# Performance work log

Hardware: AMD Instinct MI355X
Metric: run time of the kernel (lower is better)

Reference implementation:

```python
import jax, jax.numpy as jnp
import numpy as np

P_SIZE = 128   # proto_size
HID = 768      # hidden_size
BATCH = 32
NREL = 16
RATIO = 0.5    # proto_emb_ratio


def setup_inputs() -> dict:
    key = jax.random.key(0)
    k1, k2, k3, k4 = jax.random.split(key, 4)
    return {
        "instance_embedding": jax.random.normal(k1, (BATCH, HID), jnp.float32),
        # small scale keeps sigmoid(p_h @ M_r @ p_t) away from hard saturation
        "relation_embedding": jax.random.normal(k2, (NREL, HID, HID), jnp.float32) * 0.02,
        "rel_label_ids": jax.random.randint(k3, (BATCH, NREL, P_SIZE), 0, P_SIZE + 1, dtype=jnp.int32),
        "labels": jnp.arange(BATCH, dtype=jnp.int32),  # distinct -> torch.unique is exact with static shapes
        "prototypes": jax.random.normal(k4, (P_SIZE, HID), jnp.float32),  # nn.Embedding weight
    }


def reference(instance_embedding, relation_embedding, rel_label_ids, labels, prototypes):
    P, H = prototypes.shape
    B, R, _ = rel_label_ids.shape

    # torch.unique(labels, return_inverse=True): sorted uniques + inverse map.
    labels_unique = jnp.sort(labels)                      # [K] (K == B, labels distinct)
    inv = jnp.argsort(jnp.argsort(labels))                # index_list (rank of each label)
    # original code: index = index_list[k] -> rel rows permuted by inverse map
    rel_k = rel_label_ids[inv]                            # [K,R,P]

    total_nonzero = jnp.sum(rel_label_ids) > 0
    batch_mask = (jnp.sum(rel_k, axis=(1, 2)) > 0)[:, None, None]   # skip if sum(rel[index])==0
    row_mask = (jnp.sum(rel_k, axis=2) > 0)[:, :, None]             # skip if sum(rel[index][i])==0
    m = (rel_k != P) & batch_mask & row_mask & total_nonzero        # [K,R,P] active entries
    mf = m.astype(prototypes.dtype)

    P0 = prototypes                                       # get_proto_embedding(): never updated inside loop
    heads = jnp.minimum(rel_k, P - 1)                     # safe gather (masked where == P)
    Ph = P0[heads]                                        # [K,R,P,H]  (largest intermediate)
    pt = P0[labels_unique]                                # [K,H]

    # sim[k,i,j] = sigmoid(P0[head] @ M_r[i] @ P0[label_k])
    v = jnp.einsum('rhg,kg->krh', relation_embedding, pt)           # [K,R,H]
    sim = jax.nn.sigmoid(jnp.einsum('krph,krh->krp', Ph, v))        # [K,R,P]

    # logits_ol init: zeros, then logits_ol[:][:][:][0] = 1.0 sets the k==0 slab to 1.0
    base = jnp.zeros((B, R, P, 2), prototypes.dtype).at[0].set(1.0)
    l1 = jnp.where(m, sim, base[..., 1])
    l0 = jnp.where(m, 1.0 - sim, base[..., 0])
    logits_ol = jnp.stack([l0, l1], axis=-1).reshape(-1, 2)         # [K*R*P, 2]
    labels_ol = m.astype(jnp.int32).reshape(-1)                     # [K*R*P]

    # proto propagation: mean over active (i,j) of P0[head] @ M_r[i]
    w = jnp.einsum('krp,krph->krh', mf, Ph)                         # [K,R,H]
    prop = jnp.einsum('krh,rhg->kg', w, relation_embedding)         # [K,H]
    n = jnp.sum(mf, axis=(1, 2))                                    # num_prop per k
    prop = prop / jnp.maximum(n, 1.0)[:, None]
    old_rows = prototypes[labels_unique]
    new_rows = RATIO * old_rows + (1.0 - RATIO) * prop
    rows = jnp.where((n > 0)[:, None], new_rows, old_rows)
    proto_embedding = prototypes.at[labels_unique].set(rows)        # scatter update (distinct rows)

    # CrossEntropyLoss (mean); 0 when all rel ids are zero (labels_ol would be None)
    logp = jax.nn.log_softmax(logits_ol, axis=-1)
    ce = -jnp.mean(jnp.take_along_axis(logp, labels_ol[:, None], axis=1))
    loss_ol = jnp.where(total_nonzero, ce, 0.0)

    # logits = -||proto - instance||^2 pairwise: [B, P]
    diff = instance_embedding[:, None, :] - proto_embedding[None, :, :]
    logits = -jnp.sum(diff * diff, axis=2)

    return logits, loss_ol, proto_embedding
```

## Files before the change

kernel.cpp:

```cpp
#include <hip/hip_runtime.h>
#include <hip/hip_bf16.h>
#include <math.h>

#define K_B 32
#define NRELD 16
#define PSZ 128
#define HID 768

using bf16x8 = __attribute__((ext_vector_type(8))) short;
using f32x4  = __attribute__((ext_vector_type(4))) float;

__device__ __forceinline__ unsigned int f2bf(float x) {
    unsigned int u = __float_as_uint(x);
    return (u + 0x7fffu + ((u >> 16) & 1u)) >> 16;
}
__device__ __forceinline__ float bf2f(unsigned short b) {
    return __uint_as_float(((unsigned int)b) << 16);
}

__global__ __launch_bounds__(192) void k_prep(
        const int* __restrict__ labels, const int* __restrict__ relIds,
        const float* __restrict__ P0,
        unsigned short* __restrict__ S_bf, unsigned short* __restrict__ P0_bf,
        unsigned short* __restrict__ P0T_bf, unsigned short* __restrict__ pt_bf,
        int* __restrict__ rowflag, int* __restrict__ cntRow,
        int* __restrict__ done)
{
    int bid = blockIdx.x, t = threadIdx.x;
    int k = bid >> 4, r = bid & 15;
    __shared__ int lab[32], rankS[32], luS[32], ownS[128];
    __shared__ int hist[128], redS[128];
    if (t < 32) lab[t] = labels[t];
    if (t < 128) { hist[t] = 0; ownS[t] = -1; }
    __syncthreads();
    if (t < 32) { int rk = 0; for (int j = 0; j < 32; ++j) rk += (lab[j] < lab[t]); rankS[t] = rk; }
    __syncthreads();
    if (t < 32) luS[rankS[t]] = lab[t];
    __syncthreads();
    if (t < 32) ownS[luS[t]] = t;
    __syncthreads();

    int id = 0, isv = 0;
    if (t < 128) {
        id = relIds[((size_t)rankS[k]*NRELD + r)*PSZ + t];
        isv = (id != PSZ);
        if (isv) atomicAdd(&hist[id], 1);
        redS[t] = id + (isv << 20);
    }
    __syncthreads();
    for (int off = 64; off; off >>= 1) {
        if (t < off && t < 128) redS[t] += redS[t + off];
        __syncthreads();
    }
    int rowsum = redS[0] & 0xFFFFF;
    int cnt    = redS[0] >> 20;
    int rf     = (rowsum > 0);
    if (t < 128)
        S_bf[(size_t)bid*128 + t] = (unsigned short)f2bf(rf ? (float)hist[t] : 0.f);
    if (t == 0) { rowflag[bid] = rf; cntRow[bid] = cnt; }
    if (bid == 0 && t == 0) done[0] = 0;

    if (bid < 128) {
        int p = bid;
        float4 v4 = *(const float4*)&P0[(size_t)p*HID + t*4];
        unsigned int b0 = f2bf(v4.x), b1 = f2bf(v4.y), b2 = f2bf(v4.z), b3 = f2bf(v4.w);
        uint2 d; d.x = b0 | (b1 << 16); d.y = b2 | (b3 << 16);
        *(uint2*)&P0_bf[(size_t)p*HID + t*4] = d;
        P0T_bf[(size_t)(t*4+0)*128 + p] = (unsigned short)b0;
        P0T_bf[(size_t)(t*4+1)*128 + p] = (unsigned short)b1;
        P0T_bf[(size_t)(t*4+2)*128 + p] = (unsigned short)b2;
        P0T_bf[(size_t)(t*4+3)*128 + p] = (unsigned short)b3;
        int kk = ownS[p];
        if (kk >= 0) *(uint2*)&pt_bf[(size_t)kk*HID + t*4] = d;
    }
}

__global__ __launch_bounds__(256) void k_vw(
        const float* __restrict__ rel, const unsigned short* __restrict__ pt_bf,
        const unsigned short* __restrict__ S_bf, const unsigned short* __restrict__ P0T_bf,
        unsigned short* __restrict__ v_bf, unsigned short* __restrict__ w_bf,
        float* __restrict__ prop, float* __restrict__ lossAcc)
{
    __shared__ unsigned short sh[32*768 + 64*128];
    int bid = blockIdx.x, t = threadIdx.x;
    int wave = t >> 6, lane = t & 63;

    if (bid < 192) {
        int r = bid & 15, hs = bid >> 4;
        unsigned short* ptS = sh;
        unsigned short* AS  = sh + 32*768;
        for (int i = t; i < 3072; i += 256) {
            int k = i / 96, c = i % 96;
            uint4 d = *(const uint4*)&pt_bf[(size_t)k*HID + c*8];
            *(uint4*)&ptS[k*768 + (c ^ (k & 7))*8] = d;
        }
        const int gq = (t & 31) * 4;
        const int hr = t >> 5;
        const size_t relbase = ((size_t)r*HID + hs*64) * HID;
        float4 buf[8];
        #pragma unroll
        for (int rr = 0; rr < 8; ++rr)
            buf[rr] = *(const float4*)&rel[relbase + (size_t)(hr + rr*8)*HID + gq];
        f32x4 acc[2] = {{0.f,0.f,0.f,0.f},{0.f,0.f,0.f,0.f}};
        const int arow = wave*16 + (lane & 15);
        for (int gt = 0; gt < 6; ++gt) {
            __syncthreads();
            #pragma unroll
            for (int rr = 0; rr < 8; ++rr) {
                int h_l = hr + rr*8;
                float4 v4 = buf[rr];
                int cs = (gq >> 3) ^ (h_l & 7);
                uint2 d; d.x = f2bf(v4.x) | (f2bf(v4.y) << 16);
                d.y = f2bf(v4.z) | (f2bf(v4.w) << 16);
                *(uint2*)&AS[h_l*128 + cs*8 + (gq & 4)] = d;
            }
            __syncthreads();
            if (gt < 5) {
                int gn = gt*128 + 128;
                #pragma unroll
                for (int rr = 0; rr < 8; ++rr)
                    buf[rr] = *(const float4*)&rel[relbase + (size_t)(hr + rr*8)*HID + gn + gq];
            }
            #pragma unroll
            for (int kk = 0; kk < 4; ++kk) {
                int cA = (kk*4 + (lane >> 4)) ^ (arow & 7);
                bf16x8 a = *(const bf16x8*)&AS[arow*128 + cA*8];
                #pragma unroll
                for (int nf = 0; nf < 2; ++nf) {
                    int k = nf*16 + (lane & 15);
                    int cB = (gt*16 + kk*4 + (lane >> 4)) ^ (k & 7);
                    bf16x8 b = *(const bf16x8*)&ptS[k*768 + cB*8];
                    acc[nf] = __builtin_amdgcn_mfma_f32_16x16x32_bf16(a, b, acc[nf], 0, 0, 0);
                }
            }
        }
        int h_out = hs*64 + wave*16 + (lane >> 4) * 4;
        #pragma unroll
        for (int nf = 0; nf < 2; ++nf) {
            int k = nf*16 + (lane & 15);
            uint2 d; d.x = f2bf(acc[nf][0]) | (f2bf(acc[nf][1]) << 16);
            d.y = f2bf(acc[nf][2]) | (f2bf(acc[nf][3]) << 16);
            *(uint2*)&v_bf[((size_t)k*NRELD + r)*HID + h_out] = d;
        }
    } else {
        int idx = bid - 192;
        int ms = idx / 12, ns = idx % 12;
        unsigned short* AS2 = sh;
        unsigned short* BS2 = sh + 64*128;
        if (t < 64) *(float4*)&prop[idx*256 + t*4] = float4{0.f,0.f,0.f,0.f};
        if (idx == 0 && t == 0) lossAcc[0] = 0.f;
        for (int i = t; i < 1024; i += 256) {
            int row = i >> 4, c = i & 15;
            *(uint4*)&AS2[row*128 + (c ^ (row & 7))*8] =
                *(const uint4*)&S_bf[(size_t)(ms*64 + row)*128 + c*8];
            *(uint4*)&BS2[row*128 + (c ^ (row & 7))*8] =
                *(const uint4*)&P0T_bf[(size_t)(ns*64 + row)*128 + c*8];
        }
        __syncthreads();
        f32x4 acc[4] = {{0.f,0.f,0.f,0.f},{0.f,0.f,0.f,0.f},{0.f,0.f,0.f,0.f},{0.f,0.f,0.f,0.f}};
        int arow = wave*16 + (lane & 15);
        #pragma unroll
        for (int kk = 0; kk < 4; ++kk) {
            int cA = (kk*4 + (lane >> 4)) ^ (arow & 7);
            bf16x8 a = *(const bf16x8*)&AS2[arow*128 + cA*8];
            #pragma unroll
            for (int nf = 0; nf < 4; ++nf) {
                int brow = nf*16 + (lane & 15);
                int cB = (kk*4 + (lane >> 4)) ^ (brow & 7);
                bf16x8 b = *(const bf16x8*)&BS2[brow*128 + cB*8];
                acc[nf] = __builtin_amdgcn_mfma_f32_16x16x32_bf16(a, b, acc[nf], 0, 0, 0);
            }
        }
        int kr0 = ms*64 + wave*16 + (lane >> 4) * 4;
        #pragma unroll
        for (int nf = 0; nf < 4; ++nf) {
            int h = ns*64 + nf*16 + (lane & 15);
            #pragma unroll
            for (int j = 0; j < 4; ++j)
                w_bf[(size_t)(kr0 + j)*HID + h] = (unsigned short)f2bf(acc[nf][j]);
        }
    }
}

__global__ __launch_bounds__(256) void k_prop_mfma(
        const float* __restrict__ rel, const unsigned short* __restrict__ w_bf,
        float* __restrict__ prop)
{
    int r = blockIdx.x, gs = blockIdx.y, t = threadIdx.x;
    int wave = t >> 6, lane = t & 63;
    __shared__ unsigned short WS[32*768];
    __shared__ unsigned short BS[64*128];
    for (int i = t; i < 3072; i += 256) {
        int k = i / 96, c = i % 96;
        uint4 d = *(const uint4*)&w_bf[((size_t)k*NRELD + r)*HID + c*8];
        *(uint4*)&WS[k*768 + (c ^ (k & 7))*8] = d;
    }
    const int gqq = t & 15;
    const int h4  = t >> 4;
    const size_t relb = (size_t)r*HID*HID + (size_t)gs*64;
    float4 buf[8];
    #pragma unroll
    for (int sup = 0; sup < 2; ++sup)
        #pragma unroll
        for (int rr = 0; rr < 4; ++rr)
            buf[sup*4+rr] = *(const float4*)&rel[relb + (size_t)(sup*64 + h4*4 + rr)*HID + gqq*4];
    f32x4 acc[2] = {{0.f,0.f,0.f,0.f},{0.f,0.f,0.f,0.f}};
    for (int ht = 0; ht < 6; ++ht) {
        __syncthreads();
        #pragma unroll
        for (int sup = 0; sup < 2; ++sup) {
            #pragma unroll
            for (int i = 0; i < 4; ++i) {
                int g_l = gqq*4 + i;
                int hloc = sup*64 + h4*4;
                unsigned int p0 = f2bf(((const float*)&buf[sup*4+0])[i]);
                unsigned int p1 = f2bf(((const float*)&buf[sup*4+1])[i]);
                unsigned int p2 = f2bf(((const float*)&buf[sup*4+2])[i]);
                unsigned int p3 = f2bf(((const float*)&buf[sup*4+3])[i]);
                int cs = (hloc >> 3) ^ ((g_l >> 2) & 7);
                uint2 d; d.x = p0 | (p1 << 16); d.y = p2 | (p3 << 16);
                *(uint2*)&BS[g_l*128 + cs*8 + (hloc & 4)] = d;
            }
        }
        __syncthreads();
        if (ht < 5) {
            int hn = ht*128 + 128;
            #pragma unroll
            for (int sup = 0; sup < 2; ++sup)
                #pragma unroll
                for (int rr = 0; rr < 4; ++rr)
                    buf[sup*4+rr] = *(const float4*)&rel[relb + (size_t)(hn + sup*64 + h4*4 + rr)*HID + gqq*4];
        }
        int g_l = wave*16 + (lane & 15);
        #pragma unroll
        for (int kk = 0; kk < 4; ++kk) {
            int cB = (kk*4 + (lane >> 4)) ^ ((g_l >> 2) & 7);
            bf16x8 b = *(const bf16x8*)&BS[g_l*128 + cB*8];
            #pragma unroll
            for (int mf = 0; mf < 2; ++mf) {
                int arow = mf*16 + (lane & 15);
                int cA = (ht*16 + kk*4 + (lane >> 4)) ^ (arow & 7);
                bf16x8 a = *(const bf16x8*)&WS[arow*768 + cA*8];
                acc[mf] = __builtin_amdgcn_mfma_f32_16x16x32_bf16(a, b, acc[mf], 0, 0, 0);
            }
        }
    }
    int gcol = gs*64 + wave*16 + (lane & 15);
    #pragma unroll
    for (int mf = 0; mf < 2; ++mf) {
        int k0 = mf*16 + (lane >> 4)*4;
        #pragma unroll
        for (int j = 0; j < 4; ++j)
            atomicAdd(&prop[(size_t)(k0 + j)*HID + gcol], acc[mf][j]);
    }
}

__global__ __launch_bounds__(256) void k_tail(
        const unsigned short* __restrict__ v_bf, const unsigned short* __restrict__ P0_bf,
        const unsigned short* __restrict__ S_bf, float* __restrict__ lossAcc,
        int* __restrict__ done,
        const float* __restrict__ P0, const float* __restrict__ prop,
        const int* __restrict__ rowflag, const int* __restrict__ cntRow,
        const int* __restrict__ labels, const float* __restrict__ inst,
        float* __restrict__ outProto, float* __restrict__ outLogits,
        float* __restrict__ outLoss)
{
    __shared__ __align__(16) char shraw[16*772*4];
    __shared__ int lab[32], rankS[32], luS[32], ownS[128];
    __shared__ float redF[256];
    __shared__ int redI[256];
    __shared__ float nActS[16];
    __shared__ int kS2[16];
    const int bid = blockIdx.x, t = threadIdx.x;
    const int wave = t >> 6, lane = t & 63;

    if (t < 32) lab[t] = labels[t];
    if (t < 128) ownS[t] = -1;
    __syncthreads();
    if (t < 32) { int rk = 0; for (int j = 0; j < 32; ++j) rk += (lab[j] < lab[t]); rankS[t] = rk; }
    __syncthreads();
    if (t < 32) luS[rankS[t]] = lab[t];
    __syncthreads();
    if (t < 32) ownS[luS[t]] = t;
    __syncthreads();

    if (bid < 32) {
        int ms = bid;
        unsigned short* AS  = (unsigned short*)shraw;
        unsigned short* BS2 = (unsigned short*)shraw + 16*128;
        f32x4 acc[2] = {{0.f,0.f,0.f,0.f},{0.f,0.f,0.f,0.f}};
        for (int ht = 0; ht < 6; ++ht) {
            int h0 = ht * 128;
            __syncthreads();
            {
                int row = t >> 4, c = t & 15;
                *(uint4*)&AS[row*128 + (c ^ (row & 7))*8] =
                    *(const uint4*)&v_bf[(size_t)(ms*16 + row)*HID + h0 + c*8];
                #pragma unroll
                for (int q = 0; q < 8; ++q) {
                    int j2 = t + q*256;
                    int prow = j2 >> 4, c2 = j2 & 15;
                    *(uint4*)&BS2[prow*128 + (c2 ^ (prow & 7))*8] =
                        *(const uint4*)&P0_bf[(size_t)prow*HID + h0 + c2*8];
                }
            }
            __syncthreads();
            int arow = lane & 15;
            #pragma unroll
            for (int kk = 0; kk < 4; ++kk) {
                int cA = (kk*4 + (lane >> 4)) ^ (arow & 7);
                bf16x8 a = *(const bf16x8*)&AS[arow*128 + cA*8];
                #pragma unroll
                for (int nf = 0; nf < 2; ++nf) {
                    int brow = wave*32 + nf*16 + (lane & 15);
                    int cB = (kk*4 + (lane >> 4)) ^ (brow & 7);
                    bf16x8 b = *(const bf16x8*)&BS2[brow*128 + cB*8];
                    acc[nf] = __builtin_amdgcn_mfma_f32_16x16x32_bf16(a, b, acc[nf], 0, 0, 0);
                }
            }
        }
        float term = 0.f;
        #pragma unroll
        for (int nf = 0; nf < 2; ++nf) {
            int p = wave*32 + nf*16 + (lane & 15);
            int kr0 = ms*16 + (lane >> 4)*4;
            #pragma unroll
            for (int j = 0; j < 4; ++j) {
                float S = bf2f(S_bf[(size_t)(kr0 + j)*128 + p]);
                if (S != 0.f) {
                    float z = acc[nf][j];
                    float s = 1.f / (1.f + expf(-z));
                    term += S * (logf(expf(1.f - s) + expf(s)) - s);
                }
            }
        }
        redF[t] = term;
        __syncthreads();
        for (int off = 128; off; off >>= 1) {
            if (t < off) redF[t] += redF[t + off];
            __syncthreads();
        }
        if (t == 0) atomicAdd(lossAcc, redF[0]);
        __threadfence();
        __syncthreads();
        float s2 = 0.f; int tot = 0;
        #pragma unroll
        for (int q = 0; q < 2; ++q) {
            int rr2 = t + 256*q;
            int rf = rowflag[rr2];
            tot |= rf;
            if (rf) s2 += (float)cntRow[rr2];
        }
        redF[t] = s2; redI[t] = tot;
        __syncthreads();
        for (int off = 128; off; off >>= 1) {
            if (t < off) { redF[t] += redF[t + off]; redI[t] |= redI[t + off]; }
            __syncthreads();
        }
        if (t == 0) {
            int old = atomicAdd(done, 1);
            if (old == 31) {
                __threadfence();
                float cur = atomicAdd(lossAcc, 0.f);
                outLoss[0] = redI[0]
                    ? (cur + (65536.f - redF[0]) * 0.6931471805599453f) * (1.f/65536.f)
                    : 0.f;
            }
        }
    } else {
        float* protoS = (float*)shraw;
        const int PSTR = 772;
        int pb = (bid - 32) * 16;
        if (t < 16) {
            int p = pb + t;
            int k = ownS[p];
            float n = 0.f;
            if (k >= 0)
                for (int i = 0; i < 16; ++i) {
                    int rr2 = k*NRELD + i;
                    if (rowflag[rr2]) n += (float)cntRow[rr2];
                }
            nActS[t] = n; kS2[t] = k;
        }
        __syncthreads();
        for (int it = t; it < 16*192; it += 256) {
            int pl = it / 192, c = it % 192;
            int p = pb + pl;
            float4 old = *(const float4*)&P0[(size_t)p*HID + c*4];
            float4 o = old;
            int k = kS2[pl]; float n = nActS[pl];
            if (k >= 0 && n > 0.f) {
                float4 pr = *(const float4*)&prop[(size_t)k*HID + c*4];
                float invn = 0.5f / n;
                o.x = 0.5f*old.x + pr.x*invn;
                o.y = 0.5f*old.y + pr.y*invn;
                o.z = 0.5f*old.z + pr.z*invn;
                o.w = 0.5f*old.w + pr.w*invn;
            }
            *(float4*)&outProto[(size_t)p*HID + c*4] = o;
            protoS[pl*PSTR + c*4+0] = o.x;
            protoS[pl*PSTR + c*4+1] = o.y;
            protoS[pl*PSTR + c*4+2] = o.z;
            protoS[pl*PSTR + c*4+3] = o.w;
        }
        __syncthreads();
        int b = t & 31, p2 = (t >> 5) * 2;
        const float4* ir = (const float4*)&inst[(size_t)b*HID];
        float a0 = 0.f, a1 = 0.f;
        for (int q = 0; q < HID/4; ++q) {
            float4 iv = ir[q];
            float4 pv0 = *(const float4*)&protoS[p2*PSTR + q*4];
            float4 pv1 = *(const float4*)&protoS[(p2+1)*PSTR + q*4];
            float dx = iv.x - pv0.x, dy = iv.y - pv0.y, dz = iv.z - pv0.z, dw = iv.w - pv0.w;
            a0 += dx*dx + dy*dy + dz*dz + dw*dw;
            dx = iv.x - pv1.x; dy = iv.y - pv1.y; dz = iv.z - pv1.z; dw = iv.w - pv1.w;
            a1 += dx*dx + dy*dy + dz*dz + dw*dw;
        }
        outLogits[b*PSZ + pb + p2]     = -a0;
        outLogits[b*PSZ + pb + p2 + 1] = -a1;
    }
}

extern "C" void kernel_launch(void* const* d_in, const int* in_sizes, int n_in,
                              void* d_out, int out_size, void* d_ws, size_t ws_size,
                              hipStream_t stream)
{
    const float* inst  = (const float*)d_in[0];
    const float* rel   = (const float*)d_in[1];
    const int* relIds  = (const int*)d_in[2];
    const int* labels  = (const int*)d_in[3];
    const float* P0    = (const float*)d_in[4];
    float* out = (float*)d_out;
    float* outLogits = out;
    float* outLoss   = out + 4096;
    float* outProto  = out + 4097;

    char* ws = (char*)d_ws;
    unsigned short* v_bf    = (unsigned short*)(ws + 0);
    unsigned short* w_bf    = (unsigned short*)(ws + 786432);
    unsigned short* S_bf    = (unsigned short*)(ws + 1572864);
    unsigned short* P0_bf   = (unsigned short*)(ws + 1703936);
    unsigned short* P0T_bf  = (unsigned short*)(ws + 1900544);
    unsigned short* pt_bf   = (unsigned short*)(ws + 2097152);
    float* prop    = (float*)(ws + 2146304);
    float* lossAcc = (float*)(ws + 2244608);
    int*   done    = (int*)(ws + 2244736);
    int*   rowflag = (int*)(ws + 2244864);
    int*   cntRow  = (int*)(ws + 2246912);

    k_prep<<<512, 192, 0, stream>>>(labels, relIds, P0, S_bf, P0_bf, P0T_bf,
                                    pt_bf, rowflag, cntRow, done);
    k_vw<<<288, 256, 0, stream>>>(rel, pt_bf, S_bf, P0T_bf, v_bf, w_bf,
                                  prop, lossAcc);
    k_prop_mfma<<<dim3(16,12), 256, 0, stream>>>(rel, w_bf, prop);
    k_tail<<<40, 256, 0, stream>>>(v_bf, P0_bf, S_bf, lossAcc, done, P0, prop,
                                   rowflag, cntRow, labels, inst,
                                   outProto, outLogits, outLoss);
}
```

Before: 137.0 us.

## Reassociate matmuls via Y = P0·M_r so relation matrices are read once

Reorders the bilinear products: a new kernel computes Y[r] = P0 @ M_r for all 128 prototypes and reuses that tile for both the propagation sum (S^T·Y) and, in the tail, the similarity logits (Y·pt). The separate v/w kernel and the second pass over relation_embedding in k_prop_mfma are removed, so the large fp32 relation tensor is streamed once instead of twice and one launch disappears. In exchange it writes and re-reads a larger bf16 Y intermediate, and the loss stage now runs on only 16 blocks, each doing a bigger GEMM.

```diff
diff --git a/kernel.cpp b/kernel.cpp
--- a/kernel.cpp
+++ b/kernel.cpp
@@ -22,8 +22,9 @@
         const int* __restrict__ labels, const int* __restrict__ relIds,
         const float* __restrict__ P0,
         unsigned short* __restrict__ S_bf, unsigned short* __restrict__ P0_bf,
-        unsigned short* __restrict__ P0T_bf, unsigned short* __restrict__ pt_bf,
+        unsigned short* __restrict__ pt_bf,
         int* __restrict__ rowflag, int* __restrict__ cntRow,
+        float* __restrict__ prop, float* __restrict__ lossAcc,
         int* __restrict__ done)
 {
     int bid = blockIdx.x, t = threadIdx.x;
@@ -40,16 +41,15 @@
     if (t < 32) ownS[luS[t]] = t;
     __syncthreads();
 
-    int id = 0, isv = 0;
     if (t < 128) {
-        id = relIds[((size_t)rankS[k]*NRELD + r)*PSZ + t];
-        isv = (id != PSZ);
+        int id = relIds[((size_t)rankS[k]*NRELD + r)*PSZ + t];
+        int isv = (id != PSZ);
         if (isv) atomicAdd(&hist[id], 1);
         redS[t] = id + (isv << 20);
     }
     __syncthreads();
     for (int off = 64; off; off >>= 1) {
-        if (t < off && t < 128) redS[t] += redS[t + off];
+        if (t < off) redS[t] += redS[t + off];
         __syncthreads();
     }
     int rowsum = redS[0] & 0xFFFFF;
@@ -58,205 +58,148 @@
     if (t < 128)
         S_bf[(size_t)bid*128 + t] = (unsigned short)f2bf(rf ? (float)hist[t] : 0.f);
     if (t == 0) { rowflag[bid] = rf; cntRow[bid] = cnt; }
-    if (bid == 0 && t == 0) done[0] = 0;
-
+    if (bid == 0 && t == 0) { lossAcc[0] = 0.f; done[0] = 0; }
+    if (bid < 96 && t < 64) {
+        float4 z = {0.f, 0.f, 0.f, 0.f};
+        ((float4*)prop)[bid*64 + t] = z;
+    }
     if (bid < 128) {
         int p = bid;
         float4 v4 = *(const float4*)&P0[(size_t)p*HID + t*4];
         unsigned int b0 = f2bf(v4.x), b1 = f2bf(v4.y), b2 = f2bf(v4.z), b3 = f2bf(v4.w);
         uint2 d; d.x = b0 | (b1 << 16); d.y = b2 | (b3 << 16);
         *(uint2*)&P0_bf[(size_t)p*HID + t*4] = d;
-        P0T_bf[(size_t)(t*4+0)*128 + p] = (unsigned short)b0;
-        P0T_bf[(size_t)(t*4+1)*128 + p] = (unsigned short)b1;
-        P0T_bf[(size_t)(t*4+2)*128 + p] = (unsigned short)b2;
-        P0T_bf[(size_t)(t*4+3)*128 + p] = (unsigned short)b3;
         int kk = ownS[p];
         if (kk >= 0) *(uint2*)&pt_bf[(size_t)kk*HID + t*4] = d;
     }
 }
 
-__global__ __launch_bounds__(256) void k_vw(
-        const float* __restrict__ rel, const unsigned short* __restrict__ pt_bf,
-        const unsigned short* __restrict__ S_bf, const unsigned short* __restrict__ P0T_bf,
-        unsigned short* __restrict__ v_bf, unsigned short* __restrict__ w_bf,
-        float* __restrict__ prop, float* __restrict__ lossAcc)
+__global__ __launch_bounds__(256) void k_Y(
+        const float* __restrict__ rel, const unsigned short* __restrict__ P0_bf,
+        const unsigned short* __restrict__ S_bf,
+        unsigned short* __restrict__ Y_bf, float* __restrict__ prop)
 {
-    __shared__ unsigned short sh[32*768 + 64*128];
-    int bid = blockIdx.x, t = threadIdx.x;
-    int wave = t >> 6, lane = t & 63;
-
-    if (bid < 192) {
-        int r = bid & 15, hs = bid >> 4;
-        unsigned short* ptS = sh;
-        unsigned short* AS  = sh + 32*768;
-        for (int i = t; i < 3072; i += 256) {
-            int k = i / 96, c = i % 96;
-            uint4 d = *(const uint4*)&pt_bf[(size_t)k*HID + c*8];
-            *(uint4*)&ptS[k*768 + (c ^ (k & 7))*8] = d;
-        }
-        const int gq = (t & 31) * 4;
-        const int hr = t >> 5;
-        const size_t relbase = ((size_t)r*HID + hs*64) * HID;
-        float4 buf[8];
-        #pragma unroll
-        for (int rr = 0; rr < 8; ++rr)
-            buf[rr] = *(const float4*)&rel[relbase + (size_t)(hr + rr*8)*HID + gq];
-        f32x4 acc[2] = {{0.f,0.f,0.f,0.f},{0.f,0.f,0.f,0.f}};
-        const int arow = wave*16 + (lane & 15);
-        for (int gt = 0; gt < 6; ++gt) {
-            __syncthreads();
-            #pragma unroll
-            for (int rr = 0; rr < 8; ++rr) {
-                int h_l = hr + rr*8;
-                float4 v4 = buf[rr];
-                int cs = (gq >> 3) ^ (h_l & 7);
-                uint2 d; d.x = f2bf(v4.x) | (f2bf(v4.y) << 16);
-                d.y = f2bf(v4.z) | (f2bf(v4.w) << 16);
-                *(uint2*)&AS[h_l*128 + cs*8 + (gq & 4)] = d;
-            }
-            __syncthreads();
-            if (gt < 5) {
-                int gn = gt*128 + 128;
-                #pragma unroll
-                for (int rr = 0; rr < 8; ++rr)
-                    buf[rr] = *(const float4*)&rel[relbase + (size_t)(hr + rr*8)*HID + gn + gq];
-            }
-            #pragma unroll
-            for (int kk = 0; kk < 4; ++kk) {
+    __shared__ unsigned short sh[16384 + 4096];
+    unsigned short* AS  = sh;
+    unsigned short* BS  = sh + 16384;
+    unsigned short* YST = sh;
+    unsigned short* SS  = sh + 4096;
+
+    const int bid = blockIdx.x, t = threadIdx.x;
+    const int wave = t >> 6, lane = t & 63;
+    const int r = bid & 15, gs = bid >> 4;
+    const int g0 = gs * 32;
+
+    const int gq2 = t & 7;
+    const int hq  = t >> 3;
+    const size_t relb = (size_t)r*HID*HID + g0;
+
+    float4 buf[4];
+    #pragma unroll
+    for (int rr = 0; rr < 4; ++rr)
+        buf[rr] = *(const float4*)&rel[relb + (size_t)(hq*4 + rr)*HID + gq2*4];
+
+    f32x4 acc[2][2] = {{{0.f,0.f,0.f,0.f},{0.f,0.f,0.f,0.f}},
+                       {{0.f,0.f,0.f,0.f},{0.f,0.f,0.f,0.f}}};
+
+    for (int ch = 0; ch < 6; ++ch) {
+        __syncthreads();
+        #pragma unroll
+        for (int i = 0; i < 4; ++i) {
+            int g_l = gq2*4 + i;
+            int hloc = hq*4;
+            unsigned int p0 = f2bf(((const float*)&buf[0])[i]);
+            unsigned int p1 = f2bf(((const float*)&buf[1])[i]);
+            unsigned int p2 = f2bf(((const float*)&buf[2])[i]);
+            unsigned int p3 = f2bf(((const float*)&buf[3])[i]);
+            int cs = (hloc >> 3) ^ ((g_l >> 2) & 7);
+            uint2 d; d.x = p0 | (p1 << 16); d.y = p2 | (p3 << 16);
+            *(uint2*)&BS[g_l*128 + cs*8 + (hloc & 4)] = d;
+        }
+        #pragma unroll
+        for (int q = 0; q < 8; ++q) {
+            int idx = t + q*256;
+            int row = idx >> 4, c = idx & 15;
+            *(uint4*)&AS[row*128 + (c ^ (row & 7))*8] =
+                *(const uint4*)&P0_bf[(size_t)row*HID + ch*128 + c*8];
+        }
+        __syncthreads();
+        if (ch < 5) {
+            int hn = ch*128 + 128;
+            #pragma unroll
+            for (int rr = 0; rr < 4; ++rr)
+                buf[rr] = *(const float4*)&rel[relb + (size_t)(hn + hq*4 + rr)*HID + gq2*4];
+        }
+        #pragma unroll
+        for (int kk = 0; kk < 4; ++kk) {
+            #pragma unroll
+            for (int mf = 0; mf < 2; ++mf) {
+                int arow = wave*32 + mf*16 + (lane & 15);
                 int cA = (kk*4 + (lane >> 4)) ^ (arow & 7);
                 bf16x8 a = *(const bf16x8*)&AS[arow*128 + cA*8];
                 #pragma unroll
                 for (int nf = 0; nf < 2; ++nf) {
-                    int k = nf*16 + (lane & 15);
-                    int cB = (gt*16 + kk*4 + (lane >> 4)) ^ (k & 7);
-                    bf16x8 b = *(const bf16x8*)&ptS[k*768 + cB*8];
-                    acc[nf] = __builtin_amdgcn_mfma_f32_16x16x32_bf16(a, b, acc[nf], 0, 0, 0);
+                    int brow = nf*16 + (lane & 15);
+                    int cB = (kk*4 + (lane >> 4)) ^ ((brow >> 2) & 7);
+                    bf16x8 b = *(const bf16x8*)&BS[brow*128 + cB*8];
+                    acc[mf][nf] = __builtin_amdgcn_mfma_f32_16x16x32_bf16(a, b, acc[mf][nf], 0, 0, 0);
                 }
             }
         }
-        int h_out = hs*64 + wave*16 + (lane >> 4) * 4;
+    }
+    __syncthreads();
+
+    #pragma unroll
+    for (int mf = 0; mf < 2; ++mf) {
         #pragma unroll
         for (int nf = 0; nf < 2; ++nf) {
-            int k = nf*16 + (lane & 15);
-            uint2 d; d.x = f2bf(acc[nf][0]) | (f2bf(acc[nf][1]) << 16);
-            d.y = f2bf(acc[nf][2]) | (f2bf(acc[nf][3]) << 16);
-            *(uint2*)&v_bf[((size_t)k*NRELD + r)*HID + h_out] = d;
-        }
-    } else {
-        int idx = bid - 192;
-        int ms = idx / 12, ns = idx % 12;
-        unsigned short* AS2 = sh;
-        unsigned short* BS2 = sh + 64*128;
-        if (t < 64) *(float4*)&prop[idx*256 + t*4] = float4{0.f,0.f,0.f,0.f};
-        if (idx == 0 && t == 0) lossAcc[0] = 0.f;
-        for (int i = t; i < 1024; i += 256) {
-            int row = i >> 4, c = i & 15;
-            *(uint4*)&AS2[row*128 + (c ^ (row & 7))*8] =
-                *(const uint4*)&S_bf[(size_t)(ms*64 + row)*128 + c*8];
-            *(uint4*)&BS2[row*128 + (c ^ (row & 7))*8] =
-                *(const uint4*)&P0T_bf[(size_t)(ns*64 + row)*128 + c*8];
-        }
-        __syncthreads();
-        f32x4 acc[4] = {{0.f,0.f,0.f,0.f},{0.f,0.f,0.f,0.f},{0.f,0.f,0.f,0.f},{0.f,0.f,0.f,0.f}};
-        int arow = wave*16 + (lane & 15);
+            #pragma unroll
+            for (int j = 0; j < 4; ++j) {
+                int p = wave*32 + mf*16 + (lane >> 4)*4 + j;
+                int g_l = nf*16 + (lane & 15);
+                unsigned short yb = (unsigned short)f2bf(acc[mf][nf][j]);
+                Y_bf[((size_t)r*128 + p)*HID + g0 + g_l] = yb;
+                YST[g_l*128 + (((p >> 3) ^ ((g_l >> 2) & 7))*8) + (p & 7)] = yb;
+            }
+        }
+    }
+    #pragma unroll
+    for (int q = 0; q < 2; ++q) {
+        int idx = t + q*256;
+        int row = idx >> 4, c = idx & 15;
+        *(uint4*)&SS[row*128 + (c ^ (row & 7))*8] =
+            *(const uint4*)&S_bf[((size_t)row*NRELD + r)*128 + c*8];
+    }
+    __syncthreads();
+    if (wave < 2) {
+        f32x4 acc2[2] = {{0.f,0.f,0.f,0.f},{0.f,0.f,0.f,0.f}};
         #pragma unroll
         for (int kk = 0; kk < 4; ++kk) {
-            int cA = (kk*4 + (lane >> 4)) ^ (arow & 7);
-            bf16x8 a = *(const bf16x8*)&AS2[arow*128 + cA*8];
-            #pragma unroll
-            for (int nf = 0; nf < 4; ++nf) {
-                int brow = nf*16 + (lane & 15);
-                int cB = (kk*4 + (lane >> 4)) ^ (brow & 7);
-                bf16x8 b = *(const bf16x8*)&BS2[brow*128 + cB*8];
-                acc[nf] = __builtin_amdgcn_mfma_f32_16x16x32_bf16(a, b, acc[nf], 0, 0, 0);
-            }
-        }
-        int kr0 = ms*64 + wave*16 + (lane >> 4) * 4;
-        #pragma unroll
-        for (int nf = 0; nf < 4; ++nf) {
-            int h = ns*64 + nf*16 + (lane & 15);
-            #pragma unroll
-            for (int j = 0; j < 4; ++j)
-                w_bf[(size_t)(kr0 + j)*HID + h] = (unsigned short)f2bf(acc[nf][j]);
-        }
-    }
-}
-
-__global__ __launch_bounds__(256) void k_prop_mfma(
-        const float* __restrict__ rel, const unsigned short* __restrict__ w_bf,
-        float* __restrict__ prop)
-{
-    int r = blockIdx.x, gs = blockIdx.y, t = threadIdx.x;
-    int wave = t >> 6, lane = t & 63;
-    __shared__ unsigned short WS[32*768];
-    __shared__ unsigned short BS[64*128];
-    for (int i = t; i < 3072; i += 256) {
-        int k = i / 96, c = i % 96;
-        uint4 d = *(const uint4*)&w_bf[((size_t)k*NRELD + r)*HID + c*8];
-        *(uint4*)&WS[k*768 + (c ^ (k & 7))*8] = d;
-    }
-    const int gqq = t & 15;
-    const int h4  = t >> 4;
-    const size_t relb = (size_t)r*HID*HID + (size_t)gs*64;
-    float4 buf[8];
-    #pragma unroll
-    for (int sup = 0; sup < 2; ++sup)
-        #pragma unroll
-        for (int rr = 0; rr < 4; ++rr)
-            buf[sup*4+rr] = *(const float4*)&rel[relb + (size_t)(sup*64 + h4*4 + rr)*HID + gqq*4];
-    f32x4 acc[2] = {{0.f,0.f,0.f,0.f},{0.f,0.f,0.f,0.f}};
-    for (int ht = 0; ht < 6; ++ht) {
-        __syncthreads();
-        #pragma unroll
-        for (int sup = 0; sup < 2; ++sup) {
-            #pragma unroll
-            for (int i = 0; i < 4; ++i) {
-                int g_l = gqq*4 + i;
-                int hloc = sup*64 + h4*4;
-                unsigned int p0 = f2bf(((const float*)&buf[sup*4+0])[i]);
-                unsigned int p1 = f2bf(((const float*)&buf[sup*4+1])[i]);
-                unsigned int p2 = f2bf(((const float*)&buf[sup*4+2])[i]);
-                unsigned int p3 = f2bf(((const float*)&buf[sup*4+3])[i]);
-                int cs = (hloc >> 3) ^ ((g_l >> 2) & 7);
-                uint2 d; d.x = p0 | (p1 << 16); d.y = p2 | (p3 << 16);
-                *(uint2*)&BS[g_l*128 + cs*8 + (hloc & 4)] = d;
-            }
-        }
-        __syncthreads();
-        if (ht < 5) {
-            int hn = ht*128 + 128;
-            #pragma unroll
-            for (int sup = 0; sup < 2; ++sup)
-                #pragma unroll
-                for (int rr = 0; rr < 4; ++rr)
-                    buf[sup*4+rr] = *(const float4*)&rel[relb + (size_t)(hn + sup*64 + h4*4 + rr)*HID + gqq*4];
-        }
-        int g_l = wave*16 + (lane & 15);
-        #pragma unroll
-        for (int kk = 0; kk < 4; ++kk) {
-            int cB = (kk*4 + (lane >> 4)) ^ ((g_l >> 2) & 7);
-            bf16x8 b = *(const bf16x8*)&BS[g_l*128 + cB*8];
+            int brow = wave*16 + (lane & 15);
+            int cB = (kk*4 + (lane >> 4)) ^ ((brow >> 2) & 7);
+            bf16x8 b = *(const bf16x8*)&YST[brow*128 + cB*8];
             #pragma unroll
             for (int mf = 0; mf < 2; ++mf) {
                 int arow = mf*16 + (lane & 15);
-                int cA = (ht*16 + kk*4 + (lane >> 4)) ^ (arow & 7);
-                bf16x8 a = *(const bf16x8*)&WS[arow*768 + cA*8];
-                acc[mf] = __builtin_amdgcn_mfma_f32_16x16x32_bf16(a, b, acc[mf], 0, 0, 0);
-            }
-        }
-    }
-    int gcol = gs*64 + wave*16 + (lane & 15);
-    #pragma unroll
-    for (int mf = 0; mf < 2; ++mf) {
-        int k0 = mf*16 + (lane >> 4)*4;
-        #pragma unroll
-        for (int j = 0; j < 4; ++j)
-            atomicAdd(&prop[(size_t)(k0 + j)*HID + gcol], acc[mf][j]);
+                int cA = (kk*4 + (lane >> 4)) ^ (arow & 7);
+                bf16x8 a = *(const bf16x8*)&SS[arow*128 + cA*8];
+                acc2[mf] = __builtin_amdgcn_mfma_f32_16x16x32_bf16(a, b, acc2[mf], 0, 0, 0);
+            }
+        }
+        int gg = g0 + wave*16 + (lane & 15);
+        #pragma unroll
+        for (int mf = 0; mf < 2; ++mf) {
+            #pragma unroll
+            for (int j = 0; j < 4; ++j) {
+                int kkk = mf*16 + (lane >> 4)*4 + j;
+                atomicAdd(&prop[(size_t)kkk*HID + gg], acc2[mf][j]);
+            }
+        }
     }
 }
 
 __global__ __launch_bounds__(256) void k_tail(
-        const unsigned short* __restrict__ v_bf, const unsigned short* __restrict__ P0_bf,
+        const unsigned short* __restrict__ Y_bf, const unsigned short* __restrict__ pt_bf,
         const unsigned short* __restrict__ S_bf, float* __restrict__ lossAcc,
         int* __restrict__ done,
         const float* __restrict__ P0, const float* __restrict__ prop,
@@ -265,7 +208,7 @@
         float* __restrict__ outProto, float* __restrict__ outLogits,
         float* __restrict__ outLoss)
 {
-    __shared__ __align__(16) char shraw[16*772*4];
+    __shared__ __align__(16) char shraw[81920];
     __shared__ int lab[32], rankS[32], luS[32], ownS[128];
     __shared__ float redF[256];
     __shared__ int redI[256];
@@ -284,53 +227,59 @@
     if (t < 32) ownS[luS[t]] = t;
     __syncthreads();
 
-    if (bid < 32) {
-        int ms = bid;
-        unsigned short* AS  = (unsigned short*)shraw;
-        unsigned short* BS2 = (unsigned short*)shraw + 16*128;
-        f32x4 acc[2] = {{0.f,0.f,0.f,0.f},{0.f,0.f,0.f,0.f}};
-        for (int ht = 0; ht < 6; ++ht) {
-            int h0 = ht * 128;
+    if (bid < 16) {
+        const int r = bid;
+        unsigned short* ptS = (unsigned short*)shraw;
+        unsigned short* AS  = (unsigned short*)shraw + 24576;
+        for (int i = t; i < 3072; i += 256) {
+            int k = i / 96, c = i % 96;
+            uint4 d = *(const uint4*)&pt_bf[(size_t)k*HID + c*8];
+            *(uint4*)&ptS[k*768 + (c ^ (k & 7))*8] = d;
+        }
+        f32x4 acc[2][2] = {{{0.f,0.f,0.f,0.f},{0.f,0.f,0.f,0.f}},
+                           {{0.f,0.f,0.f,0.f},{0.f,0.f,0.f,0.f}}};
+        for (int ch = 0; ch < 6; ++ch) {
             __syncthreads();
-            {
-                int row = t >> 4, c = t & 15;
+            #pragma unroll
+            for (int q = 0; q < 8; ++q) {
+                int idx = t + q*256;
+                int row = idx >> 4, c = idx & 15;
                 *(uint4*)&AS[row*128 + (c ^ (row & 7))*8] =
-                    *(const uint4*)&v_bf[(size_t)(ms*16 + row)*HID + h0 + c*8];
+                    *(const uint4*)&Y_bf[((size_t)r*128 + row)*HID + ch*128 + c*8];
+            }
+            __syncthreads();
+            #pragma unroll
+            for (int kk = 0; kk < 4; ++kk) {
                 #pragma unroll
-                for (int q = 0; q < 8; ++q) {
-                    int j2 = t + q*256;
-                    int prow = j2 >> 4, c2 = j2 & 15;
-                    *(uint4*)&BS2[prow*128 + (c2 ^ (prow & 7))*8] =
-                        *(const uint4*)&P0_bf[(size_t)prow*HID + h0 + c2*8];
+                for (int mf = 0; mf < 2; ++mf) {
+                    int arow = wave*32 + mf*16 + (lane & 15);
+                    int cA = (kk*4 + (lane >> 4)) ^ (arow & 7);
+                    bf16x8 a = *(const bf16x8*)&AS[arow*128 + cA*8];
+                    #pragma unroll
+                    for (int nf = 0; nf < 2; ++nf) {
+                        int brow = nf*16 + (lane & 15);
+                        int cB = (ch*16 + kk*4 + (lane >> 4)) ^ (brow & 7);
+                        bf16x8 b = *(const bf16x8*)&ptS[brow*768 + cB*8];
+                        acc[mf][nf] = __builtin_amdgcn_mfma_f32_16x16x32_bf16(a, b, acc[mf][nf], 0, 0, 0);
+                    }
                 }
             }
-            __syncthreads();
-            int arow = lane & 15;
-            #pragma unroll
-            for (int kk = 0; kk < 4; ++kk) {
-                int cA = (kk*4 + (lane >> 4)) ^ (arow & 7);
-                bf16x8 a = *(const bf16x8*)&AS[arow*128 + cA*8];
+        }
+        float term = 0.f;
+        #pragma unroll
+        for (int mf = 0; mf < 2; ++mf) {
+            #pragma unroll
+            for (int nf = 0; nf < 2; ++nf) {
                 #pragma unroll
-                for (int nf = 0; nf < 2; ++nf) {
-                    int brow = wave*32 + nf*16 + (lane & 15);
-                    int cB = (kk*4 + (lane >> 4)) ^ (brow & 7);
-                    bf16x8 b = *(const bf16x8*)&BS2[brow*128 + cB*8];
-                    acc[nf] = __builtin_amdgcn_mfma_f32_16x16x32_bf16(a, b, acc[nf], 0, 0, 0);
-                }
-            }
-        }
-        float term = 0.f;
-        #pragma unroll
-        for (int nf = 0; nf < 2; ++nf) {
-            int p = wave*32 + nf*16 + (lane & 15);
-            int kr0 = ms*16 + (lane >> 4)*4;
-            #pragma unroll
-            for (int j = 0; j < 4; ++j) {
-                float S = bf2f(S_bf[(size_t)(kr0 + j)*128 + p]);
-                if (S != 0.f) {
-                    float z = acc[nf][j];
-                    float s = 1.f / (1.f + expf(-z));
-                    term += S * (logf(expf(1.f - s) + expf(s)) - s);
+                for (int j = 0; j < 4; ++j) {
+                    int p = wave*32 + mf*16 + (lane >> 4)*4 + j;
+                    int kkk = nf*16 + (lane & 15);
+                    float S = bf2f(S_bf[((size_t)kkk*NRELD + r)*128 + p]);
+                    if (S != 0.f) {
+                        float z = acc[mf][nf][j];
+                        float s = 1.f / (1.f + expf(-z));
+                        term += S * (logf(expf(1.f - s) + expf(s)) - s);
+                    }
                 }
             }
         }
@@ -359,7 +308,7 @@
         }
         if (t == 0) {
             int old = atomicAdd(done, 1);
-            if (old == 31) {
+            if (old == 15) {
                 __threadfence();
                 float cur = atomicAdd(lossAcc, 0.f);
                 outLoss[0] = redI[0]
@@ -370,7 +319,7 @@
     } else {
         float* protoS = (float*)shraw;
         const int PSTR = 772;
-        int pb = (bid - 32) * 16;
+        int pb = (bid - 16) * 16;
         if (t < 16) {
             int p = pb + t;
             int k = ownS[p];
@@ -436,24 +385,20 @@
     float* outProto  = out + 4097;
 
     char* ws = (char*)d_ws;
-    unsigned short* v_bf    = (unsigned short*)(ws + 0);
-    unsigned short* w_bf    = (unsigned short*)(ws + 786432);
-    unsigned short* S_bf    = (unsigned short*)(ws + 1572864);
-    unsigned short* P0_bf   = (unsigned short*)(ws + 1703936);
-    unsigned short* P0T_bf  = (unsigned short*)(ws + 1900544);
-    unsigned short* pt_bf   = (unsigned short*)(ws + 2097152);
-    float* prop    = (float*)(ws + 2146304);
-    float* lossAcc = (float*)(ws + 2244608);
-    int*   done    = (int*)(ws + 2244736);
-    int*   rowflag = (int*)(ws + 2244864);
-    int*   cntRow  = (int*)(ws + 2246912);
-
-    k_prep<<<512, 192, 0, stream>>>(labels, relIds, P0, S_bf, P0_bf, P0T_bf,
-                                    pt_bf, rowflag, cntRow, done);
-    k_vw<<<288, 256, 0, stream>>>(rel, pt_bf, S_bf, P0T_bf, v_bf, w_bf,
-                                  prop, lossAcc);
-    k_prop_mfma<<<dim3(16,12), 256, 0, stream>>>(rel, w_bf, prop);
-    k_tail<<<40, 256, 0, stream>>>(v_bf, P0_bf, S_bf, lossAcc, done, P0, prop,
+    unsigned short* Y_bf    = (unsigned short*)(ws + 0);
+    unsigned short* S_bf    = (unsigned short*)(ws + 3145728);
+    unsigned short* P0_bf   = (unsigned short*)(ws + 3276800);
+    unsigned short* pt_bf   = (unsigned short*)(ws + 3473408);
+    float* prop    = (float*)(ws + 3522560);
+    float* lossAcc = (float*)(ws + 3620864);
+    int*   done    = (int*)(ws + 3620992);
+    int*   rowflag = (int*)(ws + 3621120);
+    int*   cntRow  = (int*)(ws + 3623168);
+
+    k_prep<<<512, 192, 0, stream>>>(labels, relIds, P0, S_bf, P0_bf, pt_bf,
+                                    rowflag, cntRow, prop, lossAcc, done);
+    k_Y<<<384, 256, 0, stream>>>(rel, P0_bf, S_bf, Y_bf, prop);
+    k_tail<<<24, 256, 0, stream>>>(Y_bf, pt_bf, S_bf, lossAcc, done, P0, prop,
                                    rowflag, cntRow, labels, inst,
                                    outProto, outLogits, outLoss);
 }
```

New measurement: 129.0 us (median of 2 runs). -5.9%, faster.
